# Kernel optimization log

Hardware: AMD Instinct MI355X
Metric: run time of the kernel (lower is better)

The kernel has to match this reference:

```python
import jax, jax.numpy as jnp
import numpy as np

D_MODEL = 1024
N_HEAD = 16
D_K = D_MODEL // N_HEAD
D_FF = 4096
B, S = 4, 2048


def setup_inputs() -> dict:
    key = jax.random.key(0)
    ks = jax.random.split(key, 16)
    sd = 1.0 / np.sqrt(D_MODEL)
    sf = 1.0 / np.sqrt(D_FF)
    inp = {
        'x': jax.random.normal(ks[0], (B, S, D_MODEL), dtype=jnp.float32),
        'mask': jnp.ones((B, 1, S), dtype=jnp.int32),
        # attention projections (stored as [in, out] so y = x @ W + b)
        'wq': jax.random.normal(ks[1], (D_MODEL, D_MODEL), dtype=jnp.float32) * sd,
        'bq': jnp.zeros((D_MODEL,), dtype=jnp.float32),
        'wk': jax.random.normal(ks[2], (D_MODEL, D_MODEL), dtype=jnp.float32) * sd,
        'bk': jnp.zeros((D_MODEL,), dtype=jnp.float32),
        'wv': jax.random.normal(ks[3], (D_MODEL, D_MODEL), dtype=jnp.float32) * sd,
        'bv': jnp.zeros((D_MODEL,), dtype=jnp.float32),
        'wo': jax.random.normal(ks[4], (D_MODEL, D_MODEL), dtype=jnp.float32) * sd,
        'bo': jnp.zeros((D_MODEL,), dtype=jnp.float32),
        # feedforward
        'w1': jax.random.normal(ks[5], (D_MODEL, D_FF), dtype=jnp.float32) * sd,
        'b1': jnp.zeros((D_FF,), dtype=jnp.float32),
        'w2': jax.random.normal(ks[6], (D_FF, D_MODEL), dtype=jnp.float32) * sf,
        'b2': jnp.zeros((D_MODEL,), dtype=jnp.float32),
        # Tensor1DNorm params
        'alpha1': jnp.ones((D_MODEL,), dtype=jnp.float32),
        'bias1': jnp.zeros((D_MODEL,), dtype=jnp.float32),
        'alpha2': jnp.ones((D_MODEL,), dtype=jnp.float32),
        'bias2': jnp.zeros((D_MODEL,), dtype=jnp.float32),
    }
    return inp


def _norm(x, alpha, bias, eps=1e-6):
    # Tensor1DNorm: uses unbiased std (torch default, ddof=1), eps added to std
    mean = jnp.mean(x, axis=-1, keepdims=True)
    std = jnp.std(x, axis=-1, keepdims=True, ddof=1)
    return alpha * (x - mean) / (std + eps) + bias


def _encoder_layer(x, mask, wq, bq, wk, bk, wv, bv, wo, bo, w1, b1, w2, b2,
                   alpha1, bias1, alpha2, bias2):
    # --- self-attention sublayer (pre-norm) ---
    x2 = _norm(x, alpha1, bias1)
    Bn = x2.shape[0]
    q = (x2 @ wq + bq).reshape(Bn, -1, N_HEAD, D_K).transpose(0, 2, 1, 3)  # [B,H,S,dk]
    k = (x2 @ wk + bk).reshape(Bn, -1, N_HEAD, D_K).transpose(0, 2, 1, 3)
    v = (x2 @ wv + bv).reshape(Bn, -1, N_HEAD, D_K).transpose(0, 2, 1, 3)
    scores = jnp.einsum('bhqd,bhkd->bhqk', q, k) / jnp.sqrt(jnp.float32(D_K))
    # mask unsqueezed at dim 1 in torch: [B,1,S] -> [B,1,1,S]
    scores = jnp.where(mask[:, None, :, :] == 0, jnp.float32(-1e9), scores)
    p = jax.nn.softmax(scores, axis=-1)
    attn_out = jnp.einsum('bhqk,bhkd->bhqd', p, v)
    attn_out = attn_out.transpose(0, 2, 1, 3).reshape(Bn, -1, N_HEAD * D_K)
    x = x + (attn_out @ wo + bo)
    # --- feedforward sublayer (pre-norm) ---
    x2 = _norm(x, alpha2, bias2)
    ff = jax.nn.relu(x2 @ w1 + b1) @ w2 + b2
    return x + ff


def reference(x, mask, wq, bq, wk, bk, wv, bv, wo, bo, w1, b1, w2, b2,
              alpha1, bias1, alpha2, bias2):
    return _encoder_layer(x, mask, wq, bq, wk, bk, wv, bv, wo, bo,
                          w1, b1, w2, b2, alpha1, bias1, alpha2, bias2)
```

## Files before the change

kernel.cpp:

```cpp
#include <hip/hip_runtime.h>

#define D_MODEL 1024
#define D_FF    4096
#define N_HEADS 16
#define DK      64
#define BATCH   4
#define SEQ     2048
#define M_TOT   (BATCH*SEQ)

typedef unsigned short ushort_t;
typedef __attribute__((ext_vector_type(8))) short  short8;
typedef __attribute__((ext_vector_type(4))) float  floatx4;

__device__ __forceinline__ float bf2f(ushort_t s) {
    return __uint_as_float(((unsigned int)s) << 16);
}
__device__ __forceinline__ ushort_t f2bf(float f) {
    unsigned int u = __float_as_uint(f);
    u += 0x7fff + ((u >> 16) & 1);
    return (ushort_t)(u >> 16);
}
__device__ __forceinline__ void gll16(const void* g, void* l) {
    __builtin_amdgcn_global_load_lds(
        (const __attribute__((address_space(1))) void*)g,
        (__attribute__((address_space(3))) void*)l,
        16, 0, 0);
}

#if __has_builtin(__builtin_amdgcn_exp2f)
#define EXP2(x) __builtin_amdgcn_exp2f(x)
#else
#define EXP2(x) __expf((x) * 0.69314718055994531f)
#endif
#define L2E 1.4426950408889634f

__global__ void detect_dtype(const ushort_t* __restrict__ x, int* __restrict__ flag)
{
    const int t = threadIdx.x;
    int cnt = 0;
    for (int i = t; i < 512; i += 64) {
        ushort_t e = x[2 * i] & 0x7F80;
        cnt += (e >= 0x3800 && e <= 0x4380) ? 1 : 0;
    }
    for (int off = 32; off > 0; off >>= 1) cnt += __shfl_down(cnt, off, 64);
    if (t == 0) { flag[0] = (cnt >= 256) ? 1 : 0; flag[1] = 0; }
}

__global__ void cvt_vec_f32(const void* __restrict__ src, float* __restrict__ dst,
                            int n, float scale, const int* __restrict__ flag)
{
    const int i = blockIdx.x * 256 + threadIdx.x;
    if (i >= n) return;
    if (*flag) dst[i] = bf2f(((const ushort_t*)src)[i]) * scale;
    else       dst[i] = ((const float*)src)[i] * scale;
}

__global__ __launch_bounds__(256) void transpose_to_bf16(
    const void* __restrict__ in, ushort_t* __restrict__ out, int K, int N,
    float scale, const int* __restrict__ flag)
{
    __shared__ ushort_t tile[64 * 72];
    const int n0 = blockIdx.x * 64, k0 = blockIdx.y * 64;
    const int t = threadIdx.x, sr = t >> 2, sc = (t & 3) * 16;
    const long g = (long)(k0 + sr) * N + n0 + sc;
    ushort_t cv[16];
    if (*flag) {
        const ushort_t* p = (const ushort_t*)in;
        #pragma unroll
        for (int j = 0; j < 16; j++) cv[j] = f2bf(bf2f(p[g + j]) * scale);
    } else {
        const float* p = (const float*)in;
        #pragma unroll
        for (int j = 0; j < 16; j += 4) {
            float4 fv = *(const float4*)&p[g + j];
            cv[j] = f2bf(fv.x * scale); cv[j+1] = f2bf(fv.y * scale);
            cv[j+2] = f2bf(fv.z * scale); cv[j+3] = f2bf(fv.w * scale);
        }
    }
    #pragma unroll
    for (int j = 0; j < 16; j++) tile[sr * 72 + sc + j] = cv[j];
    __syncthreads();
    __attribute__((aligned(16))) ushort_t tmp[16];
    #pragma unroll
    for (int j = 0; j < 16; j++) tmp[j] = tile[(sc + j) * 72 + sr];
    const long go = (long)(n0 + sr) * K + k0 + sc;
    *(int4*)&out[go]     = *(const int4*)&tmp[0];
    *(int4*)&out[go + 8] = *(const int4*)&tmp[8];
}

__global__ __launch_bounds__(256) void ln_kernel(
    const void* __restrict__ xraw, const float* __restrict__ alpha,
    const float* __restrict__ beta, ushort_t* __restrict__ out,
    const int* __restrict__ flag)
{
    __shared__ float red[8];
    __shared__ float stats[2];
    const int row = blockIdx.x, t = threadIdx.x;
    const long idx = (long)row * D_MODEL + t * 4;
    float v0, v1, v2, v3;
    if (*flag) {
        ushort4 u = *(const ushort4*)&((const ushort_t*)xraw)[idx];
        v0 = bf2f(u.x); v1 = bf2f(u.y); v2 = bf2f(u.z); v3 = bf2f(u.w);
    } else {
        float4 fv = *(const float4*)&((const float*)xraw)[idx];
        v0 = fv.x; v1 = fv.y; v2 = fv.z; v3 = fv.w;
    }
    float s  = v0 + v1 + v2 + v3;
    float s2 = v0 * v0 + v1 * v1 + v2 * v2 + v3 * v3;
    for (int off = 32; off > 0; off >>= 1) {
        s  += __shfl_down(s,  off, 64);
        s2 += __shfl_down(s2, off, 64);
    }
    const int w = t >> 6, lane = t & 63;
    if (lane == 0) { red[w] = s; red[4 + w] = s2; }
    __syncthreads();
    if (t == 0) {
        float S  = red[0] + red[1] + red[2] + red[3];
        float S2 = red[4] + red[5] + red[6] + red[7];
        float mean = S / D_MODEL;
        float var  = fmaxf((S2 - mean * S) / (D_MODEL - 1), 0.f);
        stats[0] = mean;
        stats[1] = 1.f / (sqrtf(var) + 1e-6f);
    }
    __syncthreads();
    const float mean = stats[0], inv = stats[1];
    float vv[4] = {v0, v1, v2, v3};
    ushort4 o;
    ushort_t* op = (ushort_t*)&o;
    #pragma unroll
    for (int j = 0; j < 4; j++)
        op[j] = f2bf(alpha[t * 4 + j] * (vv[j] - mean) * inv + beta[t * 4 + j]);
    *(ushort4*)&out[idx] = o;
}

#define GEMM_PROLOG()                                                         \
    __shared__ ushort_t As[128 * 32];                                         \
    __shared__ ushort_t Bs[128 * 32];                                         \
    const int m0 = blockIdx.x * 128, n0 = blockIdx.y * 128;                   \
    const int t = threadIdx.x;                                                \
    const int w = t >> 6, lane = t & 63, quad = lane >> 4, l15 = lane & 15;   \
    const int wm = (w >> 1) * 64, wn = (w & 1) * 64;                          \
    floatx4 acc[4][4] = {};

#define GEMM_KLOOP(Abase, LDA, Bbase, LDB, KLEN)                              \
    {                                                                         \
    const ushort_t* gA = (Abase) + (long)(m0 + w * 32 + (lane >> 2)) * (LDA)  \
                         + (lane & 3) * 8;                                    \
    const ushort_t* gB = (Bbase) + (long)(n0 + w * 32 + (lane >> 2)) * (LDB)  \
                         + (lane & 3) * 8;                                    \
    for (int k0 = 0; k0 < (KLEN); k0 += 32) {                                 \
        gll16(gA + k0,                     &As[(w * 32) * 32]);               \
        gll16(gA + k0 + 16 * (long)(LDA), &As[(w * 32 + 16) * 32]);           \
        gll16(gB + k0,                     &Bs[(w * 32) * 32]);               \
        gll16(gB + k0 + 16 * (long)(LDB), &Bs[(w * 32 + 16) * 32]);           \
        __syncthreads();                                                      \
        short8 af[4], bf[4];                                                  \
        _Pragma("unroll")                                                     \
        for (int i = 0; i < 4; i++)                                           \
            af[i] = *(const short8*)&As[(wm + i * 16 + l15) * 32 + quad * 8]; \
        _Pragma("unroll")                                                     \
        for (int j = 0; j < 4; j++)                                           \
            bf[j] = *(const short8*)&Bs[(wn + j * 16 + l15) * 32 + quad * 8]; \
        _Pragma("unroll")                                                     \
        for (int i = 0; i < 4; i++) {                                         \
            _Pragma("unroll")                                                 \
            for (int j = 0; j < 4; j++)                                       \
                acc[i][j] = __builtin_amdgcn_mfma_f32_16x16x32_bf16(          \
                    af[i], bf[j], acc[i][j], 0, 0, 0);                        \
        }                                                                     \
        __syncthreads();                                                      \
    }                                                                         \
    }

__global__ __launch_bounds__(256) void gemm_qkv(
    const ushort_t* __restrict__ A, const ushort_t* __restrict__ BT,
    const float* __restrict__ bias, ushort_t* __restrict__ qb,
    ushort_t* __restrict__ kb, ushort_t* __restrict__ vtb, int M, int K)
{
    GEMM_PROLOG();
    GEMM_KLOOP(A, K, BT, K, K);
    const int nbase = n0 + wn;
    const int seg = nbase >> 10;
    #pragma unroll
    for (int j = 0; j < 4; j++) {
        const int ng = nbase + j * 16 + l15;
        const float bv = bias[ng];
        const int nl = ng & 1023;
        #pragma unroll
        for (int i = 0; i < 4; i++) {
            const int mb_ = m0 + wm + i * 16 + quad * 4;
            if (seg == 2) {
                ushort4 pv;
                #pragma unroll
                for (int r = 0; r < 4; r++)
                    ((ushort_t*)&pv)[r] = f2bf(acc[i][j][r] + bv);
                const long idx = ((long)(mb_ >> 11) * 1024 + nl) * 2048 + (mb_ & 2047);
                *(ushort4*)&vtb[idx] = pv;
            } else {
                ushort_t* dst = seg ? kb : qb;
                #pragma unroll
                for (int r = 0; r < 4; r++)
                    dst[(long)(mb_ + r) * 1024 + nl] = f2bf(acc[i][j][r] + bv);
            }
        }
    }
}

__global__ __launch_bounds__(256) void gemm_bias_res_trunk(
    const ushort_t* __restrict__ A, const ushort_t* __restrict__ BT,
    const float* __restrict__ bias, const void* __restrict__ res,
    float* __restrict__ C, int M, int N, int K, const int* __restrict__ flag)
{
    GEMM_PROLOG();
    const int fl = *flag;
    GEMM_KLOOP(A, K, BT, K, K);
    #pragma unroll
    for (int j = 0; j < 4; j++) {
        const int n = n0 + wn + j * 16 + l15;
        const float bv = bias[n];
        #pragma unroll
        for (int i = 0; i < 4; i++) {
            const int mbase = m0 + wm + i * 16 + quad * 4;
            #pragma unroll
            for (int r = 0; r < 4; r++) {
                const long idx = (long)(mbase + r) * N + n;
                const float rv = fl ? bf2f(((const ushort_t*)res)[idx])
                                    : ((const float*)res)[idx];
                C[idx] = acc[i][j][r] + bv + rv;
            }
        }
    }
}

__global__ __launch_bounds__(256) void gemm_relu_slice(
    const ushort_t* __restrict__ A, const ushort_t* __restrict__ BT,
    const float* __restrict__ bias, ushort_t* __restrict__ C,
    int M, int Nc, int K, int noff)
{
    GEMM_PROLOG();
    const ushort_t* BTo = BT + (long)noff * K;
    GEMM_KLOOP(A, K, BTo, K, K);
    #pragma unroll
    for (int j = 0; j < 4; j++) {
        const int n = n0 + wn + j * 16 + l15;
        const float bv = bias[noff + n];
        #pragma unroll
        for (int i = 0; i < 4; i++) {
            const int mbase = m0 + wm + i * 16 + quad * 4;
            #pragma unroll
            for (int r = 0; r < 4; r++)
                C[(long)(mbase + r) * Nc + n] = f2bf(fmaxf(acc[i][j][r] + bv, 0.f));
        }
    }
}

__global__ __launch_bounds__(256) void gemm_acc_slice(
    const ushort_t* __restrict__ A, const ushort_t* __restrict__ BT,
    const float* __restrict__ bias, float* __restrict__ C,
    int M, int N, int Kc, int koff, int Kfull, int pass0)
{
    GEMM_PROLOG();
    const ushort_t* BTo = BT + koff;
    GEMM_KLOOP(A, Kc, BTo, Kfull, Kc);
    #pragma unroll
    for (int j = 0; j < 4; j++) {
        const int n = n0 + wn + j * 16 + l15;
        const float bv = pass0 ? bias[n] : 0.f;
        #pragma unroll
        for (int i = 0; i < 4; i++) {
            const int mbase = m0 + wm + i * 16 + quad * 4;
            #pragma unroll
            for (int r = 0; r < 4; r++) {
                const long idx = (long)(mbase + r) * N + n;
                C[idx] = C[idx] + bv + acc[i][j][r];
            }
        }
    }
}

__global__ __launch_bounds__(256) void gemm_acc_final(
    const ushort_t* __restrict__ A, const ushort_t* __restrict__ BT,
    const float* __restrict__ Cin, void* __restrict__ out,
    int M, int N, int Kc, int koff, int Kfull, const int* __restrict__ flag)
{
    GEMM_PROLOG();
    const int fl = *flag;
    const ushort_t* BTo = BT + koff;
    GEMM_KLOOP(A, Kc, BTo, Kfull, Kc);
    #pragma unroll
    for (int j = 0; j < 4; j++) {
        const int n = n0 + wn + j * 16 + l15;
        #pragma unroll
        for (int i = 0; i < 4; i++) {
            const int mbase = m0 + wm + i * 16 + quad * 4;
            #pragma unroll
            for (int r = 0; r < 4; r++) {
                const long idx = (long)(mbase + r) * N + n;
                const float v = Cin[idx] + acc[i][j][r];
                if (fl) ((ushort_t*)out)[idx] = f2bf(v);
                else    ((float*)out)[idx] = v;
            }
        }
    }
}

__global__ __launch_bounds__(256) void finalize_out(
    const float* __restrict__ trunk, void* __restrict__ out,
    const int* __restrict__ flag)
{
    const long i = ((long)blockIdx.x * 256 + threadIdx.x) * 4;
    float4 tv = *(const float4*)&trunk[i];
    if (*flag) {
        ushort4 o = { f2bf(tv.x), f2bf(tv.y), f2bf(tv.z), f2bf(tv.w) };
        *(ushort4*)&((ushort_t*)out)[i] = o;
    } else {
        *(float4*)&((float*)out)[i] = tv;
    }
}

__global__ __launch_bounds__(256) void attn_kernel(
    const ushort_t* __restrict__ q, const ushort_t* __restrict__ k,
    const ushort_t* __restrict__ vt, const int* __restrict__ mask,
    ushort_t* __restrict__ out)
{
    __shared__ ushort_t Ks[64 * 72];
    __shared__ ushort_t Vs[64 * 72];
    __shared__ ushort_t Ps[128 * 72];
    __shared__ float MbL[64];
    const int qt = blockIdx.x, bh = blockIdx.y;
    const int b = bh >> 4, h = bh & 15;
    const int t = threadIdx.x, w = t >> 6, lane = t & 63;
    const int quad = lane >> 4, l15 = lane & 15;
    const int sr = t >> 2, sc = (t & 3) * 16;
    const int q0 = qt * 128;
    const long rowbase = (long)b * SEQ * D_MODEL + (long)h * DK;
    const long vtbase  = ((long)(b * 16 + h) * DK) * SEQ;

    {
        const int qr = t >> 1, qc = (t & 1) * 32;
        const long g = rowbase + (long)(q0 + qr) * D_MODEL + qc;
        *(int4*)&Ps[qr * 72 + qc]      = *(const int4*)&q[g];
        *(int4*)&Ps[qr * 72 + qc + 8]  = *(const int4*)&q[g + 8];
        *(int4*)&Ps[qr * 72 + qc + 16] = *(const int4*)&q[g + 16];
        *(int4*)&Ps[qr * 72 + qc + 24] = *(const int4*)&q[g + 24];
    }
    short8 bq[2][2];
    #pragma unroll
    for (int qg = 0; qg < 2; qg++)
        #pragma unroll
        for (int ks = 0; ks < 2; ks++)
            bq[qg][ks] = *(const short8*)&Ps[(w * 32 + qg * 16 + l15) * 72 + ks * 32 + quad * 8];

    short8 bones;
    #pragma unroll
    for (int i = 0; i < 8; i++) bones[i] = (short)0x3F80;

    floatx4 o[2][4] = {};
    floatx4 l4[2] = {};

    int4 kra, krb, vra, vrb;
    int  mreg = 0;
    {
        const long gk = rowbase + (long)sr * D_MODEL + sc;
        kra = *(const int4*)&k[gk]; krb = *(const int4*)&k[gk + 8];
        const long gv = vtbase + (long)sr * SEQ + sc;
        vra = *(const int4*)&vt[gv]; vrb = *(const int4*)&vt[gv + 8];
        if (t < 64) mreg = mask[b * SEQ + t];
    }

    for (int kt = 0; kt < SEQ / 64; kt++) {
        __syncthreads();
        *(int4*)&Ks[sr * 72 + sc]     = kra;
        *(int4*)&Ks[sr * 72 + sc + 8] = krb;
        *(int4*)&Vs[sr * 72 + sc]     = vra;
        *(int4*)&Vs[sr * 72 + sc + 8] = vrb;
        if (t < 64) MbL[t] = (mreg == 0) ? -1.0e9f : -44.0f;
        __syncthreads();
        if (kt + 1 < SEQ / 64) {
            const long gk = rowbase + (long)((kt + 1) * 64 + sr) * D_MODEL + sc;
            kra = *(const int4*)&k[gk]; krb = *(const int4*)&k[gk + 8];
            const long gv = vtbase + (long)sr * SEQ + (kt + 1) * 64 + sc;
            vra = *(const int4*)&vt[gv]; vrb = *(const int4*)&vt[gv + 8];
            if (t < 64) mreg = mask[b * SEQ + (kt + 1) * 64 + t];
        }

        floatx4 s[4][2] = {};
        __builtin_amdgcn_s_setprio(1);
        #pragma unroll
        for (int nt = 0; nt < 4; nt++) {
            short8 ak0 = *(const short8*)&Ks[(nt * 16 + l15) * 72 + quad * 8];
            s[nt][0] = __builtin_amdgcn_mfma_f32_16x16x32_bf16(ak0, bq[0][0], s[nt][0], 0, 0, 0);
            s[nt][1] = __builtin_amdgcn_mfma_f32_16x16x32_bf16(ak0, bq[1][0], s[nt][1], 0, 0, 0);
            short8 ak1 = *(const short8*)&Ks[(nt * 16 + l15) * 72 + 32 + quad * 8];
            s[nt][0] = __builtin_amdgcn_mfma_f32_16x16x32_bf16(ak1, bq[0][1], s[nt][0], 0, 0, 0);
            s[nt][1] = __builtin_amdgcn_mfma_f32_16x16x32_bf16(ak1, bq[1][1], s[nt][1], 0, 0, 0);
        }
        __builtin_amdgcn_s_setprio(0);

        #pragma unroll
        for (int qg = 0; qg < 2; qg++) {
            #pragma unroll
            for (int nt = 0; nt < 4; nt++) {
                float4 mb4 = *(const float4*)&MbL[nt * 16 + quad * 4];
                float p[4];
                #pragma unroll
                for (int r = 0; r < 4; r++)
                    p[r] = EXP2(fmaf(s[nt][qg][r], L2E, ((const float*)&mb4)[r]));
                uint2 pk;
                pk.x = __builtin_amdgcn_perm(__float_as_uint(p[1]), __float_as_uint(p[0]), 0x07060302u);
                pk.y = __builtin_amdgcn_perm(__float_as_uint(p[3]), __float_as_uint(p[2]), 0x07060302u);
                *(uint2*)&Ps[(w * 32 + qg * 16 + l15) * 72 + nt * 16 + quad * 4] = pk;
            }
        }

        __builtin_amdgcn_s_setprio(1);
        #pragma unroll
        for (int ks = 0; ks < 2; ks++) {
            short8 ap0 = *(const short8*)&Ps[(w * 32 + l15) * 72 + ks * 32 + quad * 8];
            short8 ap1 = *(const short8*)&Ps[(w * 32 + 16 + l15) * 72 + ks * 32 + quad * 8];
            #pragma unroll
            for (int j = 0; j < 4; j++) {
                short8 bv = *(const short8*)&Vs[(j * 16 + l15) * 72 + ks * 32 + quad * 8];
                o[0][j] = __builtin_amdgcn_mfma_f32_16x16x32_bf16(ap0, bv, o[0][j], 0, 0, 0);
                o[1][j] = __builtin_amdgcn_mfma_f32_16x16x32_bf16(ap1, bv, o[1][j], 0, 0, 0);
            }
            l4[0] = __builtin_amdgcn_mfma_f32_16x16x32_bf16(ap0, bones, l4[0], 0, 0, 0);
            l4[1] = __builtin_amdgcn_mfma_f32_16x16x32_bf16(ap1, bones, l4[1], 0, 0, 0);
        }
        __builtin_amdgcn_s_setprio(0);
    }
    #pragma unroll
    for (int qg = 0; qg < 2; qg++) {
        float inv[4];
        #pragma unroll
        for (int r = 0; r < 4; r++) inv[r] = 1.f / l4[qg][r];
        #pragma unroll
        for (int j = 0; j < 4; j++) {
            const int d = j * 16 + l15;
            #pragma unroll
            for (int r = 0; r < 4; r++) {
                const int row = q0 + w * 32 + qg * 16 + quad * 4 + r;
                out[rowbase + (long)row * D_MODEL + d] = f2bf(o[qg][j][r] * inv[r]);
            }
        }
    }
}

extern "C" void kernel_launch(void* const* d_in, const int* in_sizes, int n_in,
                              void* d_out, int out_size, void* d_ws, size_t ws_size,
                              hipStream_t stream)
{
    const void* x      = d_in[0];
    const int*  mask   = (const int*)d_in[1];
    const void* wq     = d_in[2];
    const void* bq     = d_in[3];
    const void* wk     = d_in[4];
    const void* bk     = d_in[5];
    const void* wv     = d_in[6];
    const void* bv     = d_in[7];
    const void* wo     = d_in[8];
    const void* bo     = d_in[9];
    const void* w1     = d_in[10];
    const void* b1     = d_in[11];
    const void* w2     = d_in[12];
    const void* b2     = d_in[13];
    const void* alpha1 = d_in[14];
    const void* bias1  = d_in[15];
    const void* alpha2 = d_in[16];
    const void* bias2  = d_in[17];

    char* ws = (char*)d_ws;
    const size_t MB = 1024 * 1024;
    const size_t KB = 1024;
    ushort_t* wqkvT = (ushort_t*)(ws + 0 * MB);
    ushort_t* woT   = (ushort_t*)(ws + 6 * MB);
    ushort_t* w1T   = (ushort_t*)(ws + 8 * MB);
    ushort_t* w2T   = (ushort_t*)(ws + 16 * MB);
    float* bqkvf = (float*)(ws + 24 * MB + 0 * 16 * KB);
    float* bof   = (float*)(ws + 24 * MB + 1 * 16 * KB);
    float* b1f   = (float*)(ws + 24 * MB + 2 * 16 * KB);
    float* b2f   = (float*)(ws + 24 * MB + 3 * 16 * KB);
    float* a1f   = (float*)(ws + 24 * MB + 4 * 16 * KB);
    float* be1f  = (float*)(ws + 24 * MB + 5 * 16 * KB);
    float* a2f   = (float*)(ws + 24 * MB + 6 * 16 * KB);
    float* be2f  = (float*)(ws + 24 * MB + 7 * 16 * KB);
    int*   flag  = (int*)(ws + 24 * MB + 8 * 16 * KB);
    int*   flagz = flag + 1;
    ushort_t* lnbuf = (ushort_t*)(ws + 25 * MB);
    ushort_t* qb    = (ushort_t*)(ws + 41 * MB);
    ushort_t* kb    = (ushort_t*)(ws + 57 * MB);
    ushort_t* vtb   = (ushort_t*)(ws + 73 * MB);
    ushort_t* attnb = lnbuf;

    const bool bigws = (ws_size >= 121ull * MB);

    dim3 blk(256);
    detect_dtype<<<1, 64, 0, stream>>>((const ushort_t*)x, flag);

    cvt_vec_f32<<<4, blk, 0, stream>>>(bq, bqkvf + 0, D_MODEL, 0.125f, flag);
    cvt_vec_f32<<<4, blk, 0, stream>>>(bk, bqkvf + 1024, D_MODEL, 1.f, flag);
    cvt_vec_f32<<<4, blk, 0, stream>>>(bv, bqkvf + 2048, D_MODEL, 1.f, flag);
    cvt_vec_f32<<<4, blk, 0, stream>>>(bo, bof, D_MODEL, 1.f, flag);
    cvt_vec_f32<<<16, blk, 0, stream>>>(b1, b1f, D_FF, 1.f, flag);
    cvt_vec_f32<<<4, blk, 0, stream>>>(b2, b2f, D_MODEL, 1.f, flag);
    cvt_vec_f32<<<4, blk, 0, stream>>>(alpha1, a1f, D_MODEL, 1.f, flag);
    cvt_vec_f32<<<4, blk, 0, stream>>>(bias1, be1f, D_MODEL, 1.f, flag);
    cvt_vec_f32<<<4, blk, 0, stream>>>(alpha2, a2f, D_MODEL, 1.f, flag);
    cvt_vec_f32<<<4, blk, 0, stream>>>(bias2, be2f, D_MODEL, 1.f, flag);

    transpose_to_bf16<<<dim3(16, 16), blk, 0, stream>>>(wq, wqkvT, D_MODEL, D_MODEL, 0.125f, flag);
    transpose_to_bf16<<<dim3(16, 16), blk, 0, stream>>>(wk, wqkvT + 1024 * 1024, D_MODEL, D_MODEL, 1.f, flag);
    transpose_to_bf16<<<dim3(16, 16), blk, 0, stream>>>(wv, wqkvT + 2048 * 1024, D_MODEL, D_MODEL, 1.f, flag);
    transpose_to_bf16<<<dim3(16, 16), blk, 0, stream>>>(wo, woT, D_MODEL, D_MODEL, 1.f, flag);
    transpose_to_bf16<<<dim3(64, 16), blk, 0, stream>>>(w1, w1T, D_MODEL, D_FF, 1.f, flag);
    transpose_to_bf16<<<dim3(16, 64), blk, 0, stream>>>(w2, w2T, D_FF, D_MODEL, 1.f, flag);

    ln_kernel<<<M_TOT, blk, 0, stream>>>(x, a1f, be1f, lnbuf, flag);

    gemm_qkv<<<dim3(64, 24), blk, 0, stream>>>(lnbuf, wqkvT, bqkvf, qb, kb, vtb,
                                               M_TOT, D_MODEL);

    attn_kernel<<<dim3(SEQ / 128, BATCH * N_HEADS), blk, 0, stream>>>(qb, kb, vtb, mask, attnb);

    if (bigws) {
        float*    trunk   = (float*)kb;
        ushort_t* ln2buf  = qb;
        ushort_t* halfbuf = (ushort_t*)(ws + 89 * MB);
        gemm_bias_res_trunk<<<dim3(64, 8), blk, 0, stream>>>(attnb, woT, bof, x, trunk,
                                                             M_TOT, D_MODEL, D_MODEL, flag);
        ln_kernel<<<M_TOT, blk, 0, stream>>>(trunk, a2f, be2f, ln2buf, flagz);
        gemm_relu_slice<<<dim3(64, 16), blk, 0, stream>>>(ln2buf, w1T, b1f, halfbuf,
                                                          M_TOT, 2048, D_MODEL, 0);
        gemm_acc_slice<<<dim3(64, 8), blk, 0, stream>>>(halfbuf, w2T, b2f, trunk,
                                                        M_TOT, D_MODEL, 2048, 0, D_FF, 1);
        gemm_relu_slice<<<dim3(64, 16), blk, 0, stream>>>(ln2buf, w1T, b1f, halfbuf,
                                                          M_TOT, 2048, D_MODEL, 2048);
        gemm_acc_final<<<dim3(64, 8), blk, 0, stream>>>(halfbuf, w2T, trunk, d_out,
                                                        M_TOT, D_MODEL, 2048, 2048, D_FF, flag);
    } else {
        float*    trunk   = (float*)qb;
        ushort_t* ln2buf  = vtb;
        ushort_t* halfbuf = lnbuf;
        gemm_bias_res_trunk<<<dim3(64, 8), blk, 0, stream>>>(attnb, woT, bof, x, trunk,
                                                             M_TOT, D_MODEL, D_MODEL, flag);
        ln_kernel<<<M_TOT, blk, 0, stream>>>(trunk, a2f, be2f, ln2buf, flagz);
        for (int qtr = 0; qtr < 4; qtr++) {
            const int off = qtr * 1024;
            gemm_relu_slice<<<dim3(64, 8), blk, 0, stream>>>(ln2buf, w1T, b1f, halfbuf,
                                                             M_TOT, 1024, D_MODEL, off);
            gemm_acc_slice<<<dim3(64, 8), blk, 0, stream>>>(halfbuf, w2T, b2f, trunk,
                                                            M_TOT, D_MODEL, 1024, off,
                                                            D_FF, qtr == 0 ? 1 : 0);
        }
        finalize_out<<<M_TOT * D_MODEL / 1024, blk, 0, stream>>>(trunk, d_out, flag);
    }
}
```

Baseline: 655.5 us.

## Double GEMM K-tile with swizzled LDS and batch parameter prep kernels

The shared GEMM k-loop now stages 64-wide K tiles instead of 32 and applies an XOR swizzle to LDS columns so fragment reads avoid bank conflicts. This halves the barriers per K step. Separately, ten vector conversion launches and four weight transposes are merged into single launches to reduce launch overhead. LDS use per block doubles, which may lower occupancy.

```diff
diff --git a/kernel.cpp b/kernel.cpp
--- a/kernel.cpp
+++ b/kernel.cpp
@@ -46,25 +46,32 @@
     if (t == 0) { flag[0] = (cnt >= 256) ? 1 : 0; flag[1] = 0; }
 }
 
-__global__ void cvt_vec_f32(const void* __restrict__ src, float* __restrict__ dst,
-                            int n, float scale, const int* __restrict__ flag)
-{
-    const int i = blockIdx.x * 256 + threadIdx.x;
-    if (i >= n) return;
-    if (*flag) dst[i] = bf2f(((const ushort_t*)src)[i]) * scale;
-    else       dst[i] = ((const float*)src)[i] * scale;
-}
-
-__global__ __launch_bounds__(256) void transpose_to_bf16(
+__global__ void cvt_params(
+    const void* bq, const void* bk, const void* bv, const void* bo,
+    const void* b1, const void* b2, const void* a1, const void* be1,
+    const void* a2, const void* be2, float* __restrict__ dst,
+    const int* __restrict__ flag)
+{
+    const int e = blockIdx.x * 256 + threadIdx.x;
+    const int seg = e >> 10;
+    const void* srcs[13] = {bq, bk, bv, bo, b1, b1, b1, b1, b2, a1, be1, a2, be2};
+    const int   base[13] = {0, 1024, 2048, 3072, 4096, 4096, 4096, 4096,
+                            8192, 9216, 10240, 11264, 12288};
+    const void* s = srcs[seg];
+    const int off = e - base[seg];
+    const float scale = (seg == 0) ? 0.125f : 1.f;
+    float v = (*flag) ? bf2f(((const ushort_t*)s)[off]) : ((const float*)s)[off];
+    dst[e] = v * scale;
+}
+
+__device__ __forceinline__ void transpose_body(
     const void* __restrict__ in, ushort_t* __restrict__ out, int K, int N,
-    float scale, const int* __restrict__ flag)
-{
-    __shared__ ushort_t tile[64 * 72];
-    const int n0 = blockIdx.x * 64, k0 = blockIdx.y * 64;
+    float scale, int fl, ushort_t* tile, int n0, int k0)
+{
     const int t = threadIdx.x, sr = t >> 2, sc = (t & 3) * 16;
     const long g = (long)(k0 + sr) * N + n0 + sc;
     ushort_t cv[16];
-    if (*flag) {
+    if (fl) {
         const ushort_t* p = (const ushort_t*)in;
         #pragma unroll
         for (int j = 0; j < 16; j++) cv[j] = f2bf(bf2f(p[g + j]) * scale);
@@ -86,6 +93,28 @@
     const long go = (long)(n0 + sr) * K + k0 + sc;
     *(int4*)&out[go]     = *(const int4*)&tmp[0];
     *(int4*)&out[go + 8] = *(const int4*)&tmp[8];
+}
+
+__global__ __launch_bounds__(256) void transpose_to_bf16(
+    const void* __restrict__ in, ushort_t* __restrict__ out, int K, int N,
+    float scale, const int* __restrict__ flag)
+{
+    __shared__ ushort_t tile[64 * 72];
+    transpose_body(in, out, K, N, scale, *flag, tile,
+                   blockIdx.x * 64, blockIdx.y * 64);
+}
+
+__global__ __launch_bounds__(256) void transpose_qkvo(
+    const void* __restrict__ wq, const void* __restrict__ wk,
+    const void* __restrict__ wv, const void* __restrict__ wo,
+    ushort_t* __restrict__ out, const int* __restrict__ flag)
+{
+    __shared__ ushort_t tile[64 * 72];
+    const int z = blockIdx.z;
+    const void* in = (z == 0) ? wq : (z == 1) ? wk : (z == 2) ? wv : wo;
+    transpose_body(in, out + (long)z * 1024 * 1024, 1024, 1024,
+                   (z == 0) ? 0.125f : 1.f, *flag, tile,
+                   blockIdx.x * 64, blockIdx.y * 64);
 }
 
 __global__ __launch_bounds__(256) void ln_kernel(
@@ -134,39 +163,46 @@
 }
 
 #define GEMM_PROLOG()                                                         \
-    __shared__ ushort_t As[128 * 32];                                         \
-    __shared__ ushort_t Bs[128 * 32];                                         \
+    __shared__ ushort_t As[128 * 64];                                         \
+    __shared__ ushort_t Bs[128 * 64];                                         \
     const int m0 = blockIdx.x * 128, n0 = blockIdx.y * 128;                   \
     const int t = threadIdx.x;                                                \
     const int w = t >> 6, lane = t & 63, quad = lane >> 4, l15 = lane & 15;   \
     const int wm = (w >> 1) * 64, wn = (w & 1) * 64;                          \
+    const int srow = lane >> 3;                         \
+    const int scol = 8 * ((lane & 7) ^ (srow & 7));     \
+    const int rswz = (l15 & 7) * 8;                        \
     floatx4 acc[4][4] = {};
 
 #define GEMM_KLOOP(Abase, LDA, Bbase, LDB, KLEN)                              \
     {                                                                         \
-    const ushort_t* gA = (Abase) + (long)(m0 + w * 32 + (lane >> 2)) * (LDA)  \
-                         + (lane & 3) * 8;                                    \
-    const ushort_t* gB = (Bbase) + (long)(n0 + w * 32 + (lane >> 2)) * (LDB)  \
-                         + (lane & 3) * 8;                                    \
-    for (int k0 = 0; k0 < (KLEN); k0 += 32) {                                 \
-        gll16(gA + k0,                     &As[(w * 32) * 32]);               \
-        gll16(gA + k0 + 16 * (long)(LDA), &As[(w * 32 + 16) * 32]);           \
-        gll16(gB + k0,                     &Bs[(w * 32) * 32]);               \
-        gll16(gB + k0 + 16 * (long)(LDB), &Bs[(w * 32 + 16) * 32]);           \
+    const ushort_t* gA = (Abase) + (long)(m0 + w * 32 + srow) * (LDA) + scol; \
+    const ushort_t* gB = (Bbase) + (long)(n0 + w * 32 + srow) * (LDB) + scol; \
+    for (int k0 = 0; k0 < (KLEN); k0 += 64) {                                 \
+        _Pragma("unroll")                                                     \
+        for (int c = 0; c < 4; c++) {                                         \
+            gll16(gA + k0 + (long)(c * 8) * (LDA), &As[(w * 32 + c * 8) * 64]);\
+            gll16(gB + k0 + (long)(c * 8) * (LDB), &Bs[(w * 32 + c * 8) * 64]);\
+        }                                                                     \
         __syncthreads();                                                      \
-        short8 af[4], bf[4];                                                  \
         _Pragma("unroll")                                                     \
-        for (int i = 0; i < 4; i++)                                           \
-            af[i] = *(const short8*)&As[(wm + i * 16 + l15) * 32 + quad * 8]; \
-        _Pragma("unroll")                                                     \
-        for (int j = 0; j < 4; j++)                                           \
-            bf[j] = *(const short8*)&Bs[(wn + j * 16 + l15) * 32 + quad * 8]; \
-        _Pragma("unroll")                                                     \
-        for (int i = 0; i < 4; i++) {                                         \
+        for (int kk = 0; kk < 2; kk++) {                                      \
+            short8 af[4], bf[4];                                              \
+            _Pragma("unroll")                                                 \
+            for (int i = 0; i < 4; i++)                                       \
+                af[i] = *(const short8*)&As[(wm + i * 16 + l15) * 64 +        \
+                        ((kk * 32 + quad * 8) ^ rswz)];                       \
             _Pragma("unroll")                                                 \
             for (int j = 0; j < 4; j++)                                       \
-                acc[i][j] = __builtin_amdgcn_mfma_f32_16x16x32_bf16(          \
-                    af[i], bf[j], acc[i][j], 0, 0, 0);                        \
+                bf[j] = *(const short8*)&Bs[(wn + j * 16 + l15) * 64 +        \
+                        ((kk * 32 + quad * 8) ^ rswz)];                       \
+            _Pragma("unroll")                                                 \
+            for (int i = 0; i < 4; i++) {                                     \
+                _Pragma("unroll")                                             \
+                for (int j = 0; j < 4; j++)                                   \
+                    acc[i][j] = __builtin_amdgcn_mfma_f32_16x16x32_bf16(      \
+                        af[i], bf[j], acc[i][j], 0, 0, 0);                    \
+            }                                                                 \
         }                                                                     \
         __syncthreads();                                                      \
     }                                                                         \
@@ -476,14 +512,15 @@
     ushort_t* woT   = (ushort_t*)(ws + 6 * MB);
     ushort_t* w1T   = (ushort_t*)(ws + 8 * MB);
     ushort_t* w2T   = (ushort_t*)(ws + 16 * MB);
-    float* bqkvf = (float*)(ws + 24 * MB + 0 * 16 * KB);
-    float* bof   = (float*)(ws + 24 * MB + 1 * 16 * KB);
-    float* b1f   = (float*)(ws + 24 * MB + 2 * 16 * KB);
-    float* b2f   = (float*)(ws + 24 * MB + 3 * 16 * KB);
-    float* a1f   = (float*)(ws + 24 * MB + 4 * 16 * KB);
-    float* be1f  = (float*)(ws + 24 * MB + 5 * 16 * KB);
-    float* a2f   = (float*)(ws + 24 * MB + 6 * 16 * KB);
-    float* be2f  = (float*)(ws + 24 * MB + 7 * 16 * KB);
+    float* pb    = (float*)(ws + 24 * MB);
+    float* bqkvf = pb + 0;
+    float* bof   = pb + 3072;
+    float* b1f   = pb + 4096;
+    float* b2f   = pb + 8192;
+    float* a1f   = pb + 9216;
+    float* be1f  = pb + 10240;
+    float* a2f   = pb + 11264;
+    float* be2f  = pb + 12288;
     int*   flag  = (int*)(ws + 24 * MB + 8 * 16 * KB);
     int*   flagz = flag + 1;
     ushort_t* lnbuf = (ushort_t*)(ws + 25 * MB);
@@ -497,21 +534,10 @@
     dim3 blk(256);
     detect_dtype<<<1, 64, 0, stream>>>((const ushort_t*)x, flag);
 
-    cvt_vec_f32<<<4, blk, 0, stream>>>(bq, bqkvf + 0, D_MODEL, 0.125f, flag);
-    cvt_vec_f32<<<4, blk, 0, stream>>>(bk, bqkvf + 1024, D_MODEL, 1.f, flag);
-    cvt_vec_f32<<<4, blk, 0, stream>>>(bv, bqkvf + 2048, D_MODEL, 1.f, flag);
-    cvt_vec_f32<<<4, blk, 0, stream>>>(bo, bof, D_MODEL, 1.f, flag);
-    cvt_vec_f32<<<16, blk, 0, stream>>>(b1, b1f, D_FF, 1.f, flag);
-    cvt_vec_f32<<<4, blk, 0, stream>>>(b2, b2f, D_MODEL, 1.f, flag);
-    cvt_vec_f32<<<4, blk, 0, stream>>>(alpha1, a1f, D_MODEL, 1.f, flag);
-    cvt_vec_f32<<<4, blk, 0, stream>>>(bias1, be1f, D_MODEL, 1.f, flag);
-    cvt_vec_f32<<<4, blk, 0, stream>>>(alpha2, a2f, D_MODEL, 1.f, flag);
-    cvt_vec_f32<<<4, blk, 0, stream>>>(bias2, be2f, D_MODEL, 1.f, flag);
-
-    transpose_to_bf16<<<dim3(16, 16), blk, 0, stream>>>(wq, wqkvT, D_MODEL, D_MODEL, 0.125f, flag);
-    transpose_to_bf16<<<dim3(16, 16), blk, 0, stream>>>(wk, wqkvT + 1024 * 1024, D_MODEL, D_MODEL, 1.f, flag);
-    transpose_to_bf16<<<dim3(16, 16), blk, 0, stream>>>(wv, wqkvT + 2048 * 1024, D_MODEL, D_MODEL, 1.f, flag);
-    transpose_to_bf16<<<dim3(16, 16), blk, 0, stream>>>(wo, woT, D_MODEL, D_MODEL, 1.f, flag);
+    cvt_params<<<52, blk, 0, stream>>>(bq, bk, bv, bo, b1, b2,
+                                       alpha1, bias1, alpha2, bias2, pb, flag);
+
+    transpose_qkvo<<<dim3(16, 16, 4), blk, 0, stream>>>(wq, wk, wv, wo, wqkvT, flag);
     transpose_to_bf16<<<dim3(64, 16), blk, 0, stream>>>(w1, w1T, D_MODEL, D_FF, 1.f, flag);
     transpose_to_bf16<<<dim3(16, 64), blk, 0, stream>>>(w2, w2T, D_FF, D_MODEL, 1.f, flag);
 
```

New measurement: 586.9 us. 10.5% less time.
